# Kernel tuning notes

Hardware: AMD Instinct MI355X
Metric: run time of the kernel (lower is better)

Reference implementation:

```python
import jax, jax.numpy as jnp
import numpy as np
from math import sqrt

P = 1.0  # axis-aligned transform exponent (init arg p)
EPS = 1e-6


def setup_inputs() -> dict:
    key = jax.random.key(0)
    k1, k2, k3, k4 = jax.random.split(key, 4)
    B, L, S, H, E = 4, 2048, 2048, 8, 64
    return {
        "queries": jax.random.normal(k1, (B, L, H, E), dtype=jnp.float32),
        "keys": jax.random.normal(k2, (B, S, H, E), dtype=jnp.float32),
        "values": jax.random.normal(k3, (B, S, H, E), dtype=jnp.float32),
        "attn_mask": jnp.zeros((1, 1, 1, 1), dtype=bool),  # unused: mask_flag=False
        "directional_weights": jnp.ones((1, 1, 1, 1), dtype=jnp.float32),
        "dynamic_param": jax.random.normal(k4, (1,), dtype=jnp.float32),
    }


def _transform(x, directional_weights, dynamic_param):
    # axis_aligned_transformation: rescale by (1/std over seq dim)^p (unbiased std, like torch)
    std = jnp.std(x, axis=-2, keepdims=True, ddof=1)
    x = x * (1.0 / (std + EPS)) ** P
    # directional_reweighting then nonlinear_mapping
    x = x * directional_weights
    return jnp.tanh(x) * dynamic_param


def reference(queries, keys, values, attn_mask, directional_weights, dynamic_param):
    B, L, H, E = queries.shape
    scale = 1.0 / sqrt(E)
    qt = _transform(queries, directional_weights, dynamic_param)  # [B,L,H,E]
    kt = _transform(keys, directional_weights, dynamic_param)     # [B,S,H,E]
    scores = jnp.einsum('blhe,bshe->bhls', qt, kt)                # [B,H,L,S]
    # per-row tau = sqrt(var(scores) + eps), unbiased variance like torch.var
    tau = jnp.sqrt(jnp.var(scores, axis=-1, keepdims=True, ddof=1) + EPS)
    A = jax.nn.softmax(scale * scores / tau, axis=-1)             # [B,H,L,S]
    V = jnp.einsum('bhls,bshd->blhd', A, values)                  # [B,L,H,D]
    return V
```

## Files before the change

### kernel.cpp

```cpp
#include <hip/hip_runtime.h>
#include <math.h>

#define B_ 4
#define L_ 2048
#define S_ 2048
#define H_ 8
#define E_ 64
#define BH_ (B_*H_)
#define EPS 1e-6f
#define LOG2E 1.44269504088896340736f

typedef __attribute__((ext_vector_type(8))) short short8;
typedef __attribute__((ext_vector_type(4))) float f32x4;

__device__ __forceinline__ unsigned short f2bf(float f) {
    unsigned int u = __float_as_uint(f);
    u = (u + 0x7fffu + ((u >> 16) & 1u)) >> 16;
    return (unsigned short)u;
}

__device__ __forceinline__ float bf2f(unsigned short u) {
    return __uint_as_float(((unsigned int)u) << 16);
}

__device__ __forceinline__ float fast_tanh(float x) {
    float e = __expf(2.0f * x);
    return 1.0f - 2.0f / (e + 1.0f);
}

__device__ __forceinline__ unsigned int cvt_pk_bf16(float lo, float hi) {
    unsigned int r;
    asm("v_cvt_pk_bf16_f32 %0, %1, %2" : "=v"(r) : "v"(lo), "v"(hi));
    return r;
}
__device__ __forceinline__ float exp2_fast(float x) {
    float r;
    asm("v_exp_f32 %0, %1" : "=v"(r) : "v"(x));
    return r;
}
__device__ __forceinline__ void swap32(unsigned int &a, unsigned int &b) {
    asm("v_permlane32_swap_b32 %0, %1" : "+v"(a), "+v"(b));
}
__device__ __forceinline__ void swap16(unsigned int &a, unsigned int &b) {
    asm("v_permlane16_swap_b32 %0, %1" : "+v"(a), "+v"(b));
}

__global__ __launch_bounds__(256) void pre_kernel(
    const float* __restrict__ xq, const float* __restrict__ xk,
    const float* __restrict__ xv,
    unsigned short* __restrict__ qt, unsigned short* __restrict__ kt,
    unsigned short* __restrict__ vt, float* __restrict__ Gf,
    const float* __restrict__ dwp, const float* __restrict__ dpp)
{
    __shared__ float ls[64][65];
    int bx = blockIdx.x;
    int tid = threadIdx.x;
    if (bx < 4096) {
        const float* x = (bx < 2048) ? xq : xk;
        unsigned short* xt = (bx < 2048) ? qt : kt;
        int wv = tid >> 6, ln = tid & 63;
        int bl = (bx & 2047) * 4 + wv;
        int b = bl >> 11, l = bl & 2047;
        const float* xb = x + (size_t)bl * 512;
        float4 fa = *(const float4*)(xb + ln * 4);
        float4 fb = *(const float4*)(xb + 256 + ln * 4);
        float s0 = fa.x + fb.x, s1 = fa.y + fb.y, s2 = fa.z + fb.z, s3 = fa.w + fb.w;
        float q0 = fa.x * fa.x + fb.x * fb.x, q1 = fa.y * fa.y + fb.y * fb.y;
        float q2 = fa.z * fa.z + fb.z * fb.z, q3 = fa.w * fa.w + fb.w * fb.w;
        s0 += __shfl_xor(s0, 16); s1 += __shfl_xor(s1, 16);
        s2 += __shfl_xor(s2, 16); s3 += __shfl_xor(s3, 16);
        q0 += __shfl_xor(q0, 16); q1 += __shfl_xor(q1, 16);
        q2 += __shfl_xor(q2, 16); q3 += __shfl_xor(q3, 16);
        s0 += __shfl_xor(s0, 32); s1 += __shfl_xor(s1, 32);
        s2 += __shfl_xor(s2, 32); s3 += __shfl_xor(s3, 32);
        q0 += __shfl_xor(q0, 32); q1 += __shfl_xor(q1, 32);
        q2 += __shfl_xor(q2, 32); q3 += __shfl_xor(q3, 32);
        float dw = dwp[0], d = dpp[0];
        auto mkw = [&](float s, float q) {
            float mean = s * 0.125f;
            float var = (q - s * mean) * (1.f / 7.f);
            var = fmaxf(var, 0.f);
            return dw / (sqrtf(var) + EPS);
        };
        float w0 = mkw(s0, q0), w1 = mkw(s1, q1), w2 = mkw(s2, q2), w3 = mkw(s3, q3);
        float ta0 = fast_tanh(fa.x * w0) * d, ta1 = fast_tanh(fa.y * w1) * d;
        float ta2 = fast_tanh(fa.z * w2) * d, ta3 = fast_tanh(fa.w * w3) * d;
        float tb0 = fast_tanh(fb.x * w0) * d, tb1 = fast_tanh(fb.y * w1) * d;
        float tb2 = fast_tanh(fb.z * w2) * d, tb3 = fast_tanh(fb.w * w3) * d;
        uint2 pa, pb;
        pa.x = cvt_pk_bf16(ta0, ta1); pa.y = cvt_pk_bf16(ta2, ta3);
        pb.x = cvt_pk_bf16(tb0, tb1); pb.y = cvt_pk_bf16(tb2, tb3);
        int hh = ln >> 4, e0 = (ln & 15) * 4;
        if (bx < 2048) {
            *(uint2*)(xt + ((size_t)(b * 8 + hh) * 2048 + l) * 64 + e0) = pa;
            *(uint2*)(xt + ((size_t)(b * 8 + hh + 4) * 2048 + l) * 64 + e0) = pb;
        } else {
            int st = l >> 6, nt = (l >> 4) & 3, mm = l & 15;
            int cc = e0 >> 5, qq = (e0 >> 3) & 3, j0 = e0 & 7;
            size_t fb0 = (size_t)(b * 8 + hh) * 131072 + st * 4096 + nt * 1024
                       + cc * 512 + qq * 128 + mm * 8 + j0;
            *(uint2*)(xt + fb0) = pa;
            *(uint2*)(xt + fb0 + (size_t)4 * 131072) = pb;
        }
    } else if (bx < 5120) {
        int t2 = bx - 4096;
        int s0 = (t2 & 31) * 64;
        int h = (t2 >> 5) & 7, b = t2 >> 8;
        int t = tid;
#pragma unroll
        for (int i = 0; i < 4; ++i) {
            int idx = t + i * 256;
            int r = idx >> 4, c4 = (idx & 15) * 4;
            const float4 f = *(const float4*)&xv[((size_t)(b * S_ + s0 + r) * H_ + h) * E_ + c4];
            ls[r][c4] = f.x; ls[r][c4 + 1] = f.y; ls[r][c4 + 2] = f.z; ls[r][c4 + 3] = f.w;
        }
        __syncthreads();
        size_t ob = ((size_t)(b * H_ + h) * (S_ / 64) + (s0 >> 6)) * 4096;
#pragma unroll
        for (int i = 0; i < 2; ++i) {
            int ri = t + i * 256;
            int et = ri >> 7, c = (ri >> 6) & 1, quad = (ri >> 4) & 3, m = ri & 15;
            int e = et * 16 + m, sb = c * 32 + quad * 8;
            uint4 u;
            u.x = cvt_pk_bf16(ls[sb + 0][e], ls[sb + 1][e]);
            u.y = cvt_pk_bf16(ls[sb + 2][e], ls[sb + 3][e]);
            u.z = cvt_pk_bf16(ls[sb + 4][e], ls[sb + 5][e]);
            u.w = cvt_pk_bf16(ls[sb + 6][e], ls[sb + 7][e]);
            *(uint4*)&vt[ob + (size_t)ri * 8] = u;
        }
    } else {
        for (int i = (bx - 5120) * 256 + tid; i < 32 * 4096 + 32 * 64; i += 32 * 256)
            Gf[i] = 0.f;
    }
}

__global__ __launch_bounds__(256) void gram_kernel(
    const unsigned short* __restrict__ kt, float* __restrict__ Gf,
    float* __restrict__ ksum)
{
    __shared__ unsigned short ks[128 * 72];
    __shared__ float gs[4096];
    int g2 = blockIdx.x;
    int bh = g2 >> 2, part = g2 & 3;
    const unsigned short* base = kt + (size_t)bh * S_ * E_ + (size_t)part * 512 * E_;
    int tid = threadIdx.x, lane = tid & 63, w = tid >> 6;
    int m = lane & 15, quad = lane >> 4;

    f32x4 acc[4][4];
#pragma unroll
    for (int i = 0; i < 4; ++i)
#pragma unroll
        for (int j = 0; j < 4; ++j) acc[i][j] = (f32x4){0.f, 0.f, 0.f, 0.f};
    float ksp[4] = {0.f, 0.f, 0.f, 0.f};

    short8 stg[4];
#pragma unroll
    for (int i = 0; i < 4; ++i)
        stg[i] = *(const short8*)(base + (size_t)(tid + i * 256) * 8);

    for (int ch = 0; ch < 4; ++ch) {
        __syncthreads();
#pragma unroll
        for (int i = 0; i < 4; ++i) {
            int u = tid + i * 256;
            int tt = u >> 9, nt = (u >> 7) & 3, cc = (u >> 6) & 1, qq = (u >> 4) & 3, mm = u & 15;
            *(short8*)&ks[(tt * 64 + nt * 16 + mm) * 72 + cc * 32 + qq * 8] = stg[i];
        }
        __syncthreads();
        if (ch < 3) {
#pragma unroll
            for (int i = 0; i < 4; ++i)
                stg[i] = *(const short8*)(base + (size_t)(ch + 1) * 8192 + (tid + i * 256) * 8);
        }
        int s0 = w * 32;
        short8 af[4];
#pragma unroll
        for (int i = 0; i < 4; ++i) {
            short8 a;
#pragma unroll
            for (int kk = 0; kk < 8; ++kk) {
                unsigned short uv = ks[(s0 + quad * 8 + kk) * 72 + i * 16 + m];
                a[kk] = (short)uv;
                ksp[i] += bf2f(uv);
            }
            af[i] = a;
        }
#pragma unroll
        for (int i = 0; i < 4; ++i)
#pragma unroll
            for (int j = 0; j < 4; ++j)
                acc[i][j] = __builtin_amdgcn_mfma_f32_16x16x32_bf16(af[i], af[j], acc[i][j], 0, 0, 0);
    }
#pragma unroll
    for (int i = 0; i < 4; ++i) {
        ksp[i] += __shfl_xor(ksp[i], 16);
        ksp[i] += __shfl_xor(ksp[i], 32);
    }
    if (lane < 16) {
#pragma unroll
        for (int i = 0; i < 4; ++i)
            atomicAdd(&ksum[bh * 64 + i * 16 + lane], ksp[i]);
    }
    for (int w2 = 0; w2 < 4; ++w2) {
        if (w == w2) {
#pragma unroll
            for (int i = 0; i < 4; ++i)
#pragma unroll
                for (int j = 0; j < 4; ++j)
#pragma unroll
                    for (int r = 0; r < 4; ++r) {
                        int idx = (i * 16 + quad * 4 + r) * 64 + j * 16 + m;
                        if (w2 == 0) gs[idx] = acc[i][j][r]; else gs[idx] += acc[i][j][r];
                    }
        }
        __syncthreads();
    }
#pragma unroll
    for (int ii = 0; ii < 16; ++ii) {
        int idx = tid + ii * 256;
        atomicAdd(&Gf[bh * 4096 + idx], gs[idx]);
    }
}

__global__ __launch_bounds__(256, 2) void attn_kernel(
    const unsigned short* __restrict__ qt,
    const unsigned short* __restrict__ ktf,
    const unsigned short* __restrict__ vt,
    const float* __restrict__ Gf,
    const float* __restrict__ ksum,
    float* __restrict__ out)
{
    __shared__ float2 ascr_s[4 * 32];
    const int tid = threadIdx.x;
    const int lane = tid & 63;
    const int w = tid >> 6;
    const int m = lane & 15;
    const int quad = lane >> 4;
    float2* ascr = ascr_s + w * 32;

    int blk = blockIdx.x;
    int bh = (blk & 7) * 4 + ((blk >> 3) & 3);
    int l0 = (blk >> 5) * 128;
    int b = bh >> 3, h = bh & 7;

    const unsigned short* qtb = qt + (size_t)bh * L_ * E_;
    const unsigned short* kb  = ktf + (size_t)bh * S_ * E_;
    const unsigned short* vtb = vt + (size_t)bh * (S_ / 64) * 4096;

    short8 qf[2][2];
#pragma unroll
    for (int g = 0; g < 2; ++g)
#pragma unroll
        for (int c = 0; c < 2; ++c)
            qf[g][c] = *(const short8*)(qtb + (size_t)(l0 + w * 32 + g * 16 + m) * E_ + c * 32 + quad * 8);

    float al2[2], nalm2[2];
    {
        const float* gb = Gf + (size_t)bh * 4096;
        short8 gfr[4][2];
#pragma unroll
        for (int j = 0; j < 4; ++j)
#pragma unroll
            for (int c = 0; c < 2; ++c) {
                const float* gp = gb + (size_t)(j * 16 + m) * 64 + c * 32 + quad * 8;
                float4 f0 = *(const float4*)gp;
                float4 f1 = *(const float4*)(gp + 4);
                uint4 u;
                u.x = cvt_pk_bf16(f0.x, f0.y); u.y = cvt_pk_bf16(f0.z, f0.w);
                u.z = cvt_pk_bf16(f1.x, f1.y); u.w = cvt_pk_bf16(f1.z, f1.w);
                gfr[j][c] = *(short8*)&u;
            }
        float ksl[4];
#pragma unroll
        for (int j = 0; j < 4; ++j) ksl[j] = ksum[bh * 64 + j * 16 + m];
#pragma unroll
        for (int g = 0; g < 2; ++g) {
            f32x4 accj[4];
#pragma unroll
            for (int j = 0; j < 4; ++j) {
                accj[j] = (f32x4){0.f, 0.f, 0.f, 0.f};
                accj[j] = __builtin_amdgcn_mfma_f32_16x16x32_bf16(qf[g][0], gfr[j][0], accj[j], 0, 0, 0);
                accj[j] = __builtin_amdgcn_mfma_f32_16x16x32_bf16(qf[g][1], gfr[j][1], accj[j], 0, 0, 0);
            }
            float ps[4] = {0, 0, 0, 0}, pr[4] = {0, 0, 0, 0};
#pragma unroll
            for (int r = 0; r < 4; ++r)
#pragma unroll
                for (int j = 0; j < 4; ++j) {
                    float qv = bf2f(qtb[(size_t)(l0 + w * 32 + g * 16 + quad * 4 + r) * E_ + j * 16 + m]);
                    ps[r] = fmaf(accj[j][r], qv, ps[r]);
                    pr[r] = fmaf(qv, ksl[j], pr[r]);
                }
#pragma unroll
            for (int mask = 1; mask < 16; mask <<= 1)
#pragma unroll
                for (int r = 0; r < 4; ++r) {
                    ps[r] += __shfl_xor(ps[r], mask);
                    pr[r] += __shfl_xor(pr[r], mask);
                }
            if (m == 0) {
#pragma unroll
                for (int r = 0; r < 4; ++r) {
                    float sum = pr[r];
                    float mu = sum * (1.f / S_);
                    float var = (ps[r] - sum * mu) * (1.f / (S_ - 1));
                    var = fmaxf(var, 0.f);
                    float tau = sqrtf(var + EPS);
                    float a = 0.125f / tau;
                    ascr[g * 16 + quad * 4 + r] = make_float2(a, a * mu);
                }
            }
        }
#pragma unroll
        for (int g = 0; g < 2; ++g) {
            float2 a2 = ascr[g * 16 + m];
            al2[g] = a2.x * LOG2E; nalm2[g] = -a2.y * LOG2E;
        }
    }

    f32x4 oacc[2][4];
#pragma unroll
    for (int g = 0; g < 2; ++g)
#pragma unroll
        for (int et = 0; et < 4; ++et) oacc[g][et] = (f32x4){0.f, 0.f, 0.f, 0.f};
    f32x4 asum2[2];
#pragma unroll
    for (int g = 0; g < 2; ++g) asum2[g] = (f32x4){0.f, 0.f, 0.f, 0.f};

    short8 ones;
#pragma unroll
    for (int j = 0; j < 8; ++j) ones[j] = (short)0x3F80;

#pragma unroll 2
    for (int st = 0; st < S_ / 64; ++st) {
        const unsigned short* kstb = kb + (size_t)st * 4096;
        const unsigned short* vstb = vtb + (size_t)st * 4096;
        short8 kf[4][2];
#pragma unroll
        for (int nt = 0; nt < 4; ++nt)
#pragma unroll
            for (int c = 0; c < 2; ++c)
                kf[nt][c] = *(const short8*)(kstb + (nt * 2 + c) * 512 + lane * 8);
        short8 vf[2][4];
#pragma unroll
        for (int c = 0; c < 2; ++c)
#pragma unroll
            for (int et = 0; et < 4; ++et)
                vf[c][et] = *(const short8*)(vstb + et * 1024 + c * 512 + lane * 8);

        unsigned int W[2][4][2];
#pragma unroll
        for (int nt = 0; nt < 4; ++nt)
#pragma unroll
            for (int g = 0; g < 2; ++g) {
                f32x4 acc = (f32x4){0.f, 0.f, 0.f, 0.f};
                acc = __builtin_amdgcn_mfma_f32_16x16x32_bf16(kf[nt][0], qf[g][0], acc, 0, 0, 0);
                acc = __builtin_amdgcn_mfma_f32_16x16x32_bf16(kf[nt][1], qf[g][1], acc, 0, 0, 0);
                float p0 = exp2_fast(fmaf(al2[g], acc[0], nalm2[g]));
                float p1 = exp2_fast(fmaf(al2[g], acc[1], nalm2[g]));
                float p2 = exp2_fast(fmaf(al2[g], acc[2], nalm2[g]));
                float p3 = exp2_fast(fmaf(al2[g], acc[3], nalm2[g]));
                W[g][nt][0] = cvt_pk_bf16(p0, p1);
                W[g][nt][1] = cvt_pk_bf16(p2, p3);
            }
#pragma unroll
        for (int g = 0; g < 2; ++g) {
            short8 pf[2];
#pragma unroll
            for (int c = 0; c < 2; ++c) {
                unsigned int a0 = W[g][2 * c][0], b0 = W[g][2 * c + 1][0];
                unsigned int a1 = W[g][2 * c][1], b1 = W[g][2 * c + 1][1];
                swap32(a0, b0); swap16(a0, b0);
                swap32(a1, b1); swap16(a1, b1);
                uint4 pk4;
                pk4.x = a0; pk4.y = a1; pk4.z = b0; pk4.w = b1;
                pf[c] = *(short8*)&pk4;
            }
#pragma unroll
            for (int et = 0; et < 4; ++et) {
                oacc[g][et] = __builtin_amdgcn_mfma_f32_16x16x32_bf16(pf[0], vf[0][et], oacc[g][et], 0, 0, 0);
                oacc[g][et] = __builtin_amdgcn_mfma_f32_16x16x32_bf16(pf[1], vf[1][et], oacc[g][et], 0, 0, 0);
            }
            asum2[g] = __builtin_amdgcn_mfma_f32_16x16x32_bf16(pf[0], ones, asum2[g], 0, 0, 0);
            asum2[g] = __builtin_amdgcn_mfma_f32_16x16x32_bf16(pf[1], ones, asum2[g], 0, 0, 0);
        }
    }

#pragma unroll
    for (int g = 0; g < 2; ++g)
#pragma unroll
        for (int r = 0; r < 4; ++r) {
            float rd = 1.0f / asum2[g][r];
            size_t row = (size_t)(b * L_ + l0 + w * 32 + g * 16 + quad * 4 + r);
#pragma unroll
            for (int et = 0; et < 4; ++et)
                out[(row * H_ + h) * E_ + et * 16 + m] = oacc[g][et][r] * rd;
        }
}

extern "C" void kernel_launch(void* const* d_in, const int* in_sizes, int n_in,
                              void* d_out, int out_size, void* d_ws, size_t ws_size,
                              hipStream_t stream)
{
    const float* q = (const float*)d_in[0];
    const float* k = (const float*)d_in[1];
    const float* v = (const float*)d_in[2];
    const float* dw = (const float*)d_in[4];
    const float* dp = (const float*)d_in[5];
    float* out = (float*)d_out;

    unsigned short* qt = (unsigned short*)d_ws;
    unsigned short* kt = qt + (size_t)BH_ * L_ * E_;
    unsigned short* vt = kt + (size_t)BH_ * S_ * E_;
    float* Gf = (float*)(vt + (size_t)BH_ * E_ * S_);
    float* ksum = Gf + (size_t)BH_ * 4096;

    pre_kernel<<<5152, 256, 0, stream>>>(q, k, v, qt, kt, vt, Gf, dw, dp);
    gram_kernel<<<128, 256, 0, stream>>>(kt, Gf, ksum);
    attn_kernel<<<512, 256, 0, stream>>>(qt, kt, vt, Gf, ksum, out);
}
```

Before: 154.2 us.

## Split key tile across wave pairs, each wave handles 64 query rows

Restructures the attention main loop so each pair of waves shares the same 64 query rows, with each wave processing half of every 64-key tile. Each wave now loads half as many K and V fragments per iteration while reusing them across four query groups instead of two, which cuts per-wave global load traffic relative to MFMA work. Partial outputs and row sums from the two halves are combined through shared memory at the end. The cost is more accumulator registers (oacc grows to 4x4), which may hurt occupancy under launch_bounds(256,2), plus an extra LDS reduction and a barrier.

New measurement: 155.7 us. Within noise of the previous version (+1.0%).

```diff
diff --git a/kernel.cpp b/kernel.cpp
--- a/kernel.cpp
+++ b/kernel.cpp
@@ -230,13 +230,17 @@
     const float* __restrict__ ksum,
     float* __restrict__ out)
 {
-    __shared__ float2 ascr_s[4 * 32];
+    __shared__ float comb[2][64][66];
+    __shared__ float dcomb[2][64];
+    __shared__ float2 ascr_s[4 * 64];
     const int tid = threadIdx.x;
     const int lane = tid & 63;
     const int w = tid >> 6;
+    const int qg = w >> 1;
+    const int sh = w & 1;
     const int m = lane & 15;
     const int quad = lane >> 4;
-    float2* ascr = ascr_s + w * 32;
+    float2* ascr = ascr_s + w * 64;
 
     int blk = blockIdx.x;
     int bh = (blk & 7) * 4 + ((blk >> 3) & 3);
@@ -247,14 +251,16 @@
     const unsigned short* kb  = ktf + (size_t)bh * S_ * E_;
     const unsigned short* vtb = vt + (size_t)bh * (S_ / 64) * 4096;
 
-    short8 qf[2][2];
-#pragma unroll
-    for (int g = 0; g < 2; ++g)
+    const int qbase = l0 + qg * 64;
+
+    short8 qf[4][2];
+#pragma unroll
+    for (int g = 0; g < 4; ++g)
 #pragma unroll
         for (int c = 0; c < 2; ++c)
-            qf[g][c] = *(const short8*)(qtb + (size_t)(l0 + w * 32 + g * 16 + m) * E_ + c * 32 + quad * 8);
-
-    float al2[2], nalm2[2];
+            qf[g][c] = *(const short8*)(qtb + (size_t)(qbase + g * 16 + m) * E_ + c * 32 + quad * 8);
+
+    float al2[4], nalm2[4];
     {
         const float* gb = Gf + (size_t)bh * 4096;
         short8 gfr[4][2];
@@ -274,7 +280,7 @@
 #pragma unroll
         for (int j = 0; j < 4; ++j) ksl[j] = ksum[bh * 64 + j * 16 + m];
 #pragma unroll
-        for (int g = 0; g < 2; ++g) {
+        for (int g = 0; g < 4; ++g) {
             f32x4 accj[4];
 #pragma unroll
             for (int j = 0; j < 4; ++j) {
@@ -287,7 +293,7 @@
             for (int r = 0; r < 4; ++r)
 #pragma unroll
                 for (int j = 0; j < 4; ++j) {
-                    float qv = bf2f(qtb[(size_t)(l0 + w * 32 + g * 16 + quad * 4 + r) * E_ + j * 16 + m]);
+                    float qv = bf2f(qtb[(size_t)(qbase + g * 16 + quad * 4 + r) * E_ + j * 16 + m]);
                     ps[r] = fmaf(accj[j][r], qv, ps[r]);
                     pr[r] = fmaf(qv, ksl[j], pr[r]);
                 }
@@ -312,20 +318,20 @@
             }
         }
 #pragma unroll
-        for (int g = 0; g < 2; ++g) {
+        for (int g = 0; g < 4; ++g) {
             float2 a2 = ascr[g * 16 + m];
             al2[g] = a2.x * LOG2E; nalm2[g] = -a2.y * LOG2E;
         }
     }
 
-    f32x4 oacc[2][4];
-#pragma unroll
-    for (int g = 0; g < 2; ++g)
+    f32x4 oacc[4][4];
+#pragma unroll
+    for (int g = 0; g < 4; ++g)
 #pragma unroll
         for (int et = 0; et < 4; ++et) oacc[g][et] = (f32x4){0.f, 0.f, 0.f, 0.f};
-    f32x4 asum2[2];
-#pragma unroll
-    for (int g = 0; g < 2; ++g) asum2[g] = (f32x4){0.f, 0.f, 0.f, 0.f};
+    f32x4 asum2[4];
+#pragma unroll
+    for (int g = 0; g < 4; ++g) asum2[g] = (f32x4){0.f, 0.f, 0.f, 0.f};
 
     short8 ones;
 #pragma unroll
@@ -333,26 +339,24 @@
 
 #pragma unroll 2
     for (int st = 0; st < S_ / 64; ++st) {
-        const unsigned short* kstb = kb + (size_t)st * 4096;
-        const unsigned short* vstb = vtb + (size_t)st * 4096;
-        short8 kf[4][2];
-#pragma unroll
-        for (int nt = 0; nt < 4; ++nt)
+        const unsigned short* kstb = kb + (size_t)st * 4096 + sh * 2048;
+        const unsigned short* vstb = vtb + (size_t)st * 4096 + sh * 512;
+        short8 kf[2][2];
+#pragma unroll
+        for (int nt = 0; nt < 2; ++nt)
 #pragma unroll
             for (int c = 0; c < 2; ++c)
                 kf[nt][c] = *(const short8*)(kstb + (nt * 2 + c) * 512 + lane * 8);
-        short8 vf[2][4];
-#pragma unroll
-        for (int c = 0; c < 2; ++c)
-#pragma unroll
-            for (int et = 0; et < 4; ++et)
-                vf[c][et] = *(const short8*)(vstb + et * 1024 + c * 512 + lane * 8);
-
-        unsigned int W[2][4][2];
-#pragma unroll
-        for (int nt = 0; nt < 4; ++nt)
-#pragma unroll
-            for (int g = 0; g < 2; ++g) {
+        short8 vf[4];
+#pragma unroll
+        for (int et = 0; et < 4; ++et)
+            vf[et] = *(const short8*)(vstb + et * 1024 + lane * 8);
+
+        unsigned int W[4][2][2];
+#pragma unroll
+        for (int nt = 0; nt < 2; ++nt)
+#pragma unroll
+            for (int g = 0; g < 4; ++g) {
                 f32x4 acc = (f32x4){0.f, 0.f, 0.f, 0.f};
                 acc = __builtin_amdgcn_mfma_f32_16x16x32_bf16(kf[nt][0], qf[g][0], acc, 0, 0, 0);
                 acc = __builtin_amdgcn_mfma_f32_16x16x32_bf16(kf[nt][1], qf[g][1], acc, 0, 0, 0);
@@ -364,38 +368,48 @@
                 W[g][nt][1] = cvt_pk_bf16(p2, p3);
             }
 #pragma unroll
-        for (int g = 0; g < 2; ++g) {
-            short8 pf[2];
-#pragma unroll
-            for (int c = 0; c < 2; ++c) {
-                unsigned int a0 = W[g][2 * c][0], b0 = W[g][2 * c + 1][0];
-                unsigned int a1 = W[g][2 * c][1], b1 = W[g][2 * c + 1][1];
-                swap32(a0, b0); swap16(a0, b0);
-                swap32(a1, b1); swap16(a1, b1);
-                uint4 pk4;
-                pk4.x = a0; pk4.y = a1; pk4.z = b0; pk4.w = b1;
-                pf[c] = *(short8*)&pk4;
-            }
-#pragma unroll
-            for (int et = 0; et < 4; ++et) {
-                oacc[g][et] = __builtin_amdgcn_mfma_f32_16x16x32_bf16(pf[0], vf[0][et], oacc[g][et], 0, 0, 0);
-                oacc[g][et] = __builtin_amdgcn_mfma_f32_16x16x32_bf16(pf[1], vf[1][et], oacc[g][et], 0, 0, 0);
-            }
-            asum2[g] = __builtin_amdgcn_mfma_f32_16x16x32_bf16(pf[0], ones, asum2[g], 0, 0, 0);
-            asum2[g] = __builtin_amdgcn_mfma_f32_16x16x32_bf16(pf[1], ones, asum2[g], 0, 0, 0);
-        }
-    }
-
-#pragma unroll
-    for (int g = 0; g < 2; ++g)
-#pragma unroll
-        for (int r = 0; r < 4; ++r) {
-            float rd = 1.0f / asum2[g][r];
-            size_t row = (size_t)(b * L_ + l0 + w * 32 + g * 16 + quad * 4 + r);
+        for (int g = 0; g < 4; ++g) {
+            unsigned int a0 = W[g][0][0], b0 = W[g][1][0];
+            unsigned int a1 = W[g][0][1], b1 = W[g][1][1];
+            swap32(a0, b0); swap16(a0, b0);
+            swap32(a1, b1); swap16(a1, b1);
+            uint4 pk4;
+            pk4.x = a0; pk4.y = a1; pk4.z = b0; pk4.w = b1;
+            short8 pf = *(short8*)&pk4;
 #pragma unroll
             for (int et = 0; et < 4; ++et)
-                out[(row * H_ + h) * E_ + et * 16 + m] = oacc[g][et][r] * rd;
-        }
+                oacc[g][et] = __builtin_amdgcn_mfma_f32_16x16x32_bf16(pf, vf[et], oacc[g][et], 0, 0, 0);
+            asum2[g] = __builtin_amdgcn_mfma_f32_16x16x32_bf16(pf, ones, asum2[g], 0, 0, 0);
+        }
+    }
+
+    if (sh == 1) {
+#pragma unroll
+        for (int g = 0; g < 4; ++g)
+#pragma unroll
+            for (int r = 0; r < 4; ++r) {
+                int row = g * 16 + quad * 4 + r;
+                if (m == 0) dcomb[qg][row] = asum2[g][r];
+#pragma unroll
+                for (int et = 0; et < 4; ++et)
+                    comb[qg][row][et * 16 + m] = oacc[g][et][r];
+            }
+    }
+    __syncthreads();
+    if (sh == 0) {
+#pragma unroll
+        for (int g = 0; g < 4; ++g)
+#pragma unroll
+            for (int r = 0; r < 4; ++r) {
+                int row = g * 16 + quad * 4 + r;
+                float rd = 1.0f / (asum2[g][r] + dcomb[qg][row]);
+                size_t grow = (size_t)(b * L_ + qbase + row);
+#pragma unroll
+                for (int et = 0; et < 4; ++et)
+                    out[(grow * H_ + h) * E_ + et * 16 + m] =
+                        (oacc[g][et][r] + comb[qg][row][et * 16 + m]) * rd;
+            }
+    }
 }
 
 extern "C" void kernel_launch(void* const* d_in, const int* in_sizes, int n_in,
```
